# Optimization experiments

Hardware: AMD Instinct MI355X
Metric: run time of the kernel (lower is better)

Reference implementation:

```python
import jax, jax.numpy as jnp
import numpy as np

IN_CH, HID_CH = 32, 64
DILS = (1, 2, 4)


def _conv(x, w, b, dil, pad):
    # x: [B,C,H,W], w: [O,I,kh,kw]
    y = jax.lax.conv_general_dilated(
        x, w, window_strides=(1, 1), padding=[(pad, pad), (pad, pad)],
        rhs_dilation=(dil, dil), dimension_numbers=("NCHW", "OIHW", "NCHW"))
    return y + b[None, :, None, None]


def setup_inputs() -> dict:
    key = jax.random.key(0)
    ks = jax.random.split(key, 9)
    x_seq = jax.random.normal(ks[0], (4, 16, IN_CH, 64, 64), dtype=jnp.float32)
    params = {}
    ch = IN_CH
    for li, _ in enumerate(DILS):
        fan_in = (ch + HID_CH) * 9
        scale = 1.0 / np.sqrt(fan_in)
        params[f"gw{li}"] = jax.random.normal(ks[1 + 2 * li], (4 * HID_CH, ch + HID_CH, 3, 3), jnp.float32) * scale
        params[f"gb{li}"] = jnp.zeros((4 * HID_CH,), jnp.float32)
        ch = HID_CH
    # layer 0 residual 1x1 projection (in_ch != hid_ch)
    params["rw0"] = jax.random.normal(ks[7], (HID_CH, IN_CH, 1, 1), jnp.float32) * (1.0 / np.sqrt(IN_CH))
    params["rb0"] = jnp.zeros((HID_CH,), jnp.float32)
    return {"x_seq": x_seq, **params}


def _run_layer(seq, gw, gb, dil, res_fn):
    # seq: [B,T,C,H,W]
    B, T, C, H, W = seq.shape
    h0 = jnp.zeros((B, HID_CH, H, W), seq.dtype)
    c0 = jnp.zeros_like(h0)

    def step(carry, xt):
        h, c = carry
        g = _conv(jnp.concatenate([xt, h], axis=1), gw, gb, dil, dil)
        i, f, gg, o = jnp.split(g, 4, axis=1)
        c_new = jax.nn.sigmoid(f) * c + jax.nn.sigmoid(i) * jnp.tanh(gg)
        h_new = jax.nn.sigmoid(o) * jnp.tanh(c_new)
        h_out = h_new + res_fn(xt)  # residual added BEFORE next-step carry (matches torch)
        return (h_out, c_new), h_out

    xs = jnp.moveaxis(seq, 1, 0)  # [T,B,C,H,W]
    _, ys = jax.lax.scan(step, (h0, c0), xs)
    return jnp.moveaxis(ys, 0, 1)  # [B,T,hid,H,W]


def reference(x_seq, gw0, gb0, gw1, gb1, gw2, gb2, rw0, rb0):
    res0 = lambda xt: _conv(xt, rw0, rb0, 1, 0)
    ident = lambda xt: xt
    out = _run_layer(x_seq, gw0, gb0, DILS[0], res0)
    out = _run_layer(out, gw1, gb1, DILS[1], ident)
    out = _run_layer(out, gw2, gb2, DILS[2], ident)
    return out
```

## Files before the change

kernel.cpp:

```cpp
#include <hip/hip_runtime.h>
#include <hip/hip_bf16.h>

typedef __bf16 bf16;
typedef __bf16 bf16x8 __attribute__((ext_vector_type(8)));
typedef float f32x4 __attribute__((ext_vector_type(4)));
typedef unsigned short u16;
typedef unsigned short u16x8 __attribute__((ext_vector_type(8)));

#define TT 16
#define BB 4
#define HH 64
#define WW 64
#define HID 64

__device__ __forceinline__ float sigm_f(float x) { return 1.f / (1.f + __expf(-x)); }
__device__ __forceinline__ float tanh_f(float x) { return 1.f - 2.f / (__expf(2.f * x) + 1.f); }

__global__ void xpose_kernel(const float* __restrict__ x, bf16* __restrict__ xb) {
  int idx = blockIdx.x * blockDim.x + threadIdx.x;
  const int total = TT * BB * HH * WW * 32;
  if (idx >= total) return;
  int c = idx & 31;
  int xx = (idx >> 5) & 63;
  int y = (idx >> 11) & 63;
  int b = (idx >> 17) & 3;
  int t = idx >> 19;
  float v = x[((((b * TT + t) * 32 + c) * HH + y) * WW + xx)];
  xb[idx] = (bf16)v;
}

template <int CIN>
__global__ void wprep_kernel(const float* __restrict__ gw, bf16* __restrict__ bmat,
                             const float* __restrict__ rw, bf16* __restrict__ rwb) {
  const int K = CIN * 9;
  int idx = blockIdx.x * blockDim.x + threadIdx.x;
  int total = 256 * K;
  if (idx < total) {
    int n = idx / K;
    int kk = idx - n * K;
    int half = n >> 7, j = n & 127, gate = j >> 5, hcl = j & 31;
    int o = gate * 64 + half * 32 + hcl;
    int tap = kk / CIN, c = kk - tap * CIN;
    int ky = tap / 3, kx = tap - ky * 3;
    float v = gw[((o * CIN + c) * 3 + ky) * 3 + kx];
    int kt = kk >> 5, kin = kk & 31;
    bmat[(kt * 256 + n) * 32 + kin] = (bf16)v;
  } else if (rw != nullptr) {
    int r = idx - total;
    if (r < 64 * 32) rwb[r] = (bf16)rw[r];
  }
}

template <int L>
__global__ __launch_bounds__(512) void step_kernel(
    const bf16* __restrict__ xsrc, bf16* __restrict__ hbuf,
    const bf16* __restrict__ bmat, const float* __restrict__ gb,
    float* __restrict__ cbuf, const bf16* __restrict__ rwb,
    const float* __restrict__ rb, float* __restrict__ dout, int t) {
  constexpr int Cx = (L == 0) ? 32 : 64;
  constexpr int C = Cx + 64;
  constexpr int DIL = (L == 0) ? 1 : (L == 1 ? 2 : 4);
  constexpr int Wp = WW + 2 * DIL;
  constexpr int KT = (9 * C) / 32;
  constexpr int CT = C / 32;
  constexpr int HS = (L == 2) ? 2 : 16;

  __shared__ __align__(16) char smem[3 * Wp * C * 2 + 2 * 16384];
  char* alds = smem;
  char* blds = smem + 3 * Wp * C * 2;

  int bid = blockIdx.x;
  int b = bid >> 6, y = bid & 63;
  int tid = threadIdx.x;

  struct Bregs { u16x8 lo, hi; };
  auto loadB = [&](int kt) {
    Bregs r;
    const bf16* src = bmat + (size_t)kt * 256 * 32;
    r.lo = *(const u16x8*)(src + (size_t)tid * 8);
    r.hi = *(const u16x8*)(src + (size_t)(tid + 512) * 8);
    return r;
  };
  auto writeB = [&](const Bregs& r, int kt) {
    char* dst = blds + (kt & 1) * 16384;
    {
      int j = tid;
      int n = j >> 2, kin8 = (j & 3) * 8;
      int off = (n * 32 + kin8) * 2;
      off ^= (n & 7) << 4;
      *(u16x8*)(dst + off) = r.lo;
    }
    {
      int j = tid + 512;
      int n = j >> 2, kin8 = (j & 3) * 8;
      int off = (n * 32 + kin8) * 2;
      off ^= (n & 7) << 4;
      *(u16x8*)(dst + off) = r.hi;
    }
  };

  Bregs breg = loadB(0);

  {
    const int chunks = 3 * Wp * (C / 8);
    for (int i = tid; i < chunks; i += 512) {
      int cg = i % (C / 8);
      int rem = i / (C / 8);
      int col = rem % Wp;
      int row3 = rem / Wp;
      int c = cg * 8;
      int xs = col - DIL;
      int ys = y + (row3 - 1) * DIL;
      u16x8 v = {0, 0, 0, 0, 0, 0, 0, 0};
      if ((unsigned)xs < 64u && (unsigned)ys < 64u) {
        if (c < Cx) {
          v = *(const u16x8*)(xsrc + (size_t)(((t * BB + b) * HH + ys) * WW + xs) * Cx + c);
        } else if (t > 0) {
          int slot = (t - 1) & (HS - 1);
          v = *(const u16x8*)(hbuf + (size_t)(((slot * BB + b) * HH + ys) * WW + xs) * 64 + (c - Cx));
        }
      }
      int off = ((row3 * Wp + col) * C + c) * 2;
      off ^= (col & 7) << 4;
      *(u16x8*)(alds + off) = v;
    }
  }

  writeB(breg, 0);
  if (KT > 1) breg = loadB(1);

  int lane = tid & 63;
  int wave = tid >> 6;
  int pxg = wave & 3, half = wave >> 2;
  int pxbase = pxg * 16;
  int l15 = lane & 15, kgrp = lane >> 4;

  f32x4 acc[8];
  #pragma unroll
  for (int i = 0; i < 8; ++i) acc[i] = f32x4{0.f, 0.f, 0.f, 0.f};

  for (int kt = 0; kt < KT; ++kt) {
    __syncthreads();
    if (kt + 1 < KT) {
      writeB(breg, kt + 1);
      if (kt + 2 < KT) breg = loadB(kt + 2);
    }
    int tap = kt / CT;
    int cb = (kt % CT) * 32;
    int ky = tap / 3, kx = tap - ky * 3;
    int col = pxbase + l15 + kx * DIL;
    int aoff = ((ky * Wp + col) * C + cb + kgrp * 8) * 2;
    aoff ^= (col & 7) << 4;
    bf16x8 af = *(const bf16x8*)(alds + aoff);
    const char* bbase = blds + (kt & 1) * 16384;
    #pragma unroll
    for (int nt = 0; nt < 8; ++nt) {
      int n = half * 128 + nt * 16 + l15;
      int boff = (n * 32 + kgrp * 8) * 2;
      boff ^= (n & 7) << 4;
      bf16x8 bfr = *(const bf16x8*)(bbase + boff);
      acc[nt] = __builtin_amdgcn_mfma_f32_16x16x32_bf16(af, bfr, acc[nt], 0, 0, 0);
    }
  }

  #pragma unroll
  for (int hcu = 0; hcu < 2; ++hcu) {
    int hc = half * 32 + hcu * 16 + l15;
    float bi = gb[hc], bfg = gb[64 + hc], bgg = gb[128 + hc], bog = gb[192 + hc];
    f32x4 vi = acc[0 + hcu], vf = acc[2 + hcu], vg = acc[4 + hcu], vo = acc[6 + hcu];

    float rwv[32];
    float rbv = 0.f;
    if constexpr (L == 0) {
      rbv = rb[hc];
      const u16x8* rp = (const u16x8*)(rwb + hc * 32);
      #pragma unroll
      for (int q = 0; q < 4; ++q) {
        bf16x8 wb = *(const bf16x8*)(rp + q);
        #pragma unroll
        for (int e = 0; e < 8; ++e) rwv[q * 8 + e] = (float)wb[e];
      }
    }

    #pragma unroll
    for (int r = 0; r < 4; ++r) {
      int px = pxbase + kgrp * 4 + r;
      float giv = sigm_f(vi[r] + bi);
      float gfv = sigm_f(vf[r] + bfg);
      float ggv = tanh_f(vg[r] + bgg);
      float gov = sigm_f(vo[r] + bog);
      int cidx = ((b * HH + y) * WW + px) * 64 + hc;
      float cold = (t > 0) ? cbuf[cidx] : 0.f;
      float cn = gfv * cold + giv * ggv;
      cbuf[cidx] = cn;
      float hn = gov * tanh_f(cn);

      float res;
      int colc = px + DIL;
      if constexpr (L == 0) {
        float s = rbv;
        #pragma unroll
        for (int q = 0; q < 4; ++q) {
          int off = (((1 * Wp + colc) * C + q * 8) * 2) ^ ((colc & 7) << 4);
          bf16x8 xv = *(const bf16x8*)(alds + off);
          #pragma unroll
          for (int e = 0; e < 8; ++e) s += rwv[q * 8 + e] * (float)xv[e];
        }
        res = s;
      } else {
        int off = (((1 * Wp + colc) * C + hc) * 2) ^ ((colc & 7) << 4);
        res = (float)*(const bf16*)(alds + off);
      }
      float ho = hn + res;
      int hslot = t & (HS - 1);
      hbuf[(size_t)(((hslot * BB + b) * HH + y) * WW + px) * 64 + hc] = (bf16)ho;
      if constexpr (L == 2) {
        dout[(size_t)(((b * TT + t) * HID + hc) * HH + y) * WW + px] = ho;
      }
    }
  }
}

extern "C" void kernel_launch(void* const* d_in, const int* in_sizes, int n_in,
                              void* d_out, int out_size, void* d_ws, size_t ws_size,
                              hipStream_t stream) {
  const float* x_seq = (const float*)d_in[0];
  const float* gw0 = (const float*)d_in[1];
  const float* gb0 = (const float*)d_in[2];
  const float* gw1 = (const float*)d_in[3];
  const float* gb1 = (const float*)d_in[4];
  const float* gw2 = (const float*)d_in[5];
  const float* gb2 = (const float*)d_in[6];
  const float* rw0 = (const float*)d_in[7];
  const float* rb0 = (const float*)d_in[8];
  float* dout = (float*)d_out;

  char* ws = (char*)d_ws;
  size_t off = 0;
  auto carve = [&](size_t bytes) {
    char* p = ws + off;
    off += (bytes + 255) & ~(size_t)255;
    return p;
  };
  bf16* xb0 = (bf16*)carve((size_t)TT * BB * HH * WW * 32 * 2);
  bf16* seqA = (bf16*)carve((size_t)TT * BB * HH * WW * 64 * 2);
  bf16* seqB = (bf16*)carve((size_t)TT * BB * HH * WW * 64 * 2);
  bf16* hC = (bf16*)carve((size_t)2 * BB * HH * WW * 64 * 2);
  float* cbuf = (float*)carve((size_t)BB * HH * WW * 64 * 4);
  bf16* bm0 = (bf16*)carve((size_t)27 * 256 * 32 * 2);
  bf16* bm1 = (bf16*)carve((size_t)36 * 256 * 32 * 2);
  bf16* bm2 = (bf16*)carve((size_t)36 * 256 * 32 * 2);
  bf16* rwb = (bf16*)carve((size_t)64 * 32 * 2);

  {
    int total = TT * BB * HH * WW * 32;
    xpose_kernel<<<(total + 255) / 256, 256, 0, stream>>>(x_seq, xb0);
  }
  {
    int total = 256 * 96 * 9 + 64 * 32;
    wprep_kernel<96><<<(total + 255) / 256, 256, 0, stream>>>(gw0, bm0, rw0, rwb);
  }
  {
    int total = 256 * 128 * 9;
    wprep_kernel<128><<<(total + 255) / 256, 256, 0, stream>>>(gw1, bm1, nullptr, nullptr);
    wprep_kernel<128><<<(total + 255) / 256, 256, 0, stream>>>(gw2, bm2, nullptr, nullptr);
  }

  for (int t = 0; t < TT; ++t)
    step_kernel<0><<<BB * HH, 512, 0, stream>>>(xb0, seqA, bm0, gb0, cbuf, rwb, rb0, nullptr, t);
  for (int t = 0; t < TT; ++t)
    step_kernel<1><<<BB * HH, 512, 0, stream>>>(seqA, seqB, bm1, gb1, cbuf, nullptr, nullptr, nullptr, t);
  for (int t = 0; t < TT; ++t)
    step_kernel<2><<<BB * HH, 512, 0, stream>>>(seqB, hC, bm2, gb2, cbuf, nullptr, nullptr, dout, t);
}
```

Before: 1.262 ms.

## Keep gate weights in registers and restructure MFMA tiling per wave

Weight tiles are no longer staged through LDS with a barrier per k-step. Each wave now streams its own slice of B directly from global memory into a four-deep register ring, which removes the per-iteration __syncthreads. The wave tiling changes to two pixel M-tiles by four gate N-tiles, so each B fragment is reused across two MFMAs. The activation LDS layout is reorganized into 32-channel slabs, launch bounds request two blocks per CU, and the layer-2 output store is vectorized. In exchange, B is reloaded from global/L2 by every wave and register pressure rises.

```diff
diff --git a/kernel.cpp b/kernel.cpp
--- a/kernel.cpp
+++ b/kernel.cpp
@@ -38,8 +38,8 @@
   if (idx < total) {
     int n = idx / K;
     int kk = idx - n * K;
-    int half = n >> 7, j = n & 127, gate = j >> 5, hcl = j & 31;
-    int o = gate * 64 + half * 32 + hcl;
+    int q = n >> 6, j = n & 63, g = j >> 4, hcl = j & 15;
+    int o = g * 64 + q * 16 + hcl;
     int tap = kk / CIN, c = kk - tap * CIN;
     int ky = tap / 3, kx = tap - ky * 3;
     float v = gw[((o * CIN + c) * 3 + ky) * 3 + kx];
@@ -52,7 +52,7 @@
 }
 
 template <int L>
-__global__ __launch_bounds__(512) void step_kernel(
+__global__ __launch_bounds__(512, 2) void step_kernel(
     const bf16* __restrict__ xsrc, bf16* __restrict__ hbuf,
     const bf16* __restrict__ bmat, const float* __restrict__ gb,
     float* __restrict__ cbuf, const bf16* __restrict__ rwb,
@@ -65,50 +65,36 @@
   constexpr int CT = C / 32;
   constexpr int HS = (L == 2) ? 2 : 16;
 
-  __shared__ __align__(16) char smem[3 * Wp * C * 2 + 2 * 16384];
-  char* alds = smem;
-  char* blds = smem + 3 * Wp * C * 2;
+  __shared__ __align__(16) char alds[CT * 3 * Wp * 64];
 
   int bid = blockIdx.x;
   int b = bid >> 6, y = bid & 63;
   int tid = threadIdx.x;
-
-  struct Bregs { u16x8 lo, hi; };
-  auto loadB = [&](int kt) {
-    Bregs r;
-    const bf16* src = bmat + (size_t)kt * 256 * 32;
-    r.lo = *(const u16x8*)(src + (size_t)tid * 8);
-    r.hi = *(const u16x8*)(src + (size_t)(tid + 512) * 8);
-    return r;
+  int lane = tid & 63, wave = tid >> 6;
+  int l15 = lane & 15, kgrp = lane >> 4;
+  int pxg = wave >> 2, q = wave & 3;
+
+  const char* bmat_c = (const char*)bmat;
+  const int voffB = q * 4096 + l15 * 64 + kgrp * 16;
+
+  bf16x8 bfr[4][4];
+  auto loadB = [&](int slot, int kt) {
+    #pragma unroll
+    for (int g = 0; g < 4; ++g)
+      bfr[slot][g] = *(const bf16x8*)(bmat_c + (size_t)kt * 16384 + voffB + g * 1024);
   };
-  auto writeB = [&](const Bregs& r, int kt) {
-    char* dst = blds + (kt & 1) * 16384;
-    {
-      int j = tid;
-      int n = j >> 2, kin8 = (j & 3) * 8;
-      int off = (n * 32 + kin8) * 2;
-      off ^= (n & 7) << 4;
-      *(u16x8*)(dst + off) = r.lo;
-    }
-    {
-      int j = tid + 512;
-      int n = j >> 2, kin8 = (j & 3) * 8;
-      int off = (n * 32 + kin8) * 2;
-      off ^= (n & 7) << 4;
-      *(u16x8*)(dst + off) = r.hi;
-    }
-  };
-
-  Bregs breg = loadB(0);
+  loadB(0, 0);
+  loadB(1, 1);
 
   {
     const int chunks = 3 * Wp * (C / 8);
     for (int i = tid; i < chunks; i += 512) {
-      int cg = i % (C / 8);
-      int rem = i / (C / 8);
-      int col = rem % Wp;
-      int row3 = rem / Wp;
+      int col = i % Wp;
+      int rem = i / Wp;
+      int row3 = rem % 3;
+      int cg = rem / 3;
       int c = cg * 8;
+      int j = cg >> 2, sub = cg & 3;
       int xs = col - DIL;
       int ys = y + (row3 - 1) * DIL;
       u16x8 v = {0, 0, 0, 0, 0, 0, 0, 0};
@@ -120,71 +106,67 @@
           v = *(const u16x8*)(hbuf + (size_t)(((slot * BB + b) * HH + ys) * WW + xs) * 64 + (c - Cx));
         }
       }
-      int off = ((row3 * Wp + col) * C + c) * 2;
+      int off = ((j * 3 + row3) * Wp + col) * 64 + sub * 16;
       off ^= (col & 7) << 4;
       *(u16x8*)(alds + off) = v;
     }
   }
-
-  writeB(breg, 0);
-  if (KT > 1) breg = loadB(1);
-
-  int lane = tid & 63;
-  int wave = tid >> 6;
-  int pxg = wave & 3, half = wave >> 2;
-  int pxbase = pxg * 16;
-  int l15 = lane & 15, kgrp = lane >> 4;
-
-  f32x4 acc[8];
-  #pragma unroll
-  for (int i = 0; i < 8; ++i) acc[i] = f32x4{0.f, 0.f, 0.f, 0.f};
-
+  __syncthreads();
+
+  int abase[2][3];
+  #pragma unroll
+  for (int m = 0; m < 2; ++m)
+    #pragma unroll
+    for (int kx = 0; kx < 3; ++kx) {
+      int col = pxg * 32 + m * 16 + l15 + kx * DIL;
+      abase[m][kx] = (col * 64 + kgrp * 16) ^ ((col & 7) << 4);
+    }
+
+  f32x4 acc[2][4];
+  #pragma unroll
+  for (int m = 0; m < 2; ++m)
+    #pragma unroll
+    for (int g = 0; g < 4; ++g) acc[m][g] = f32x4{0.f, 0.f, 0.f, 0.f};
+
+  #pragma unroll
   for (int kt = 0; kt < KT; ++kt) {
-    __syncthreads();
-    if (kt + 1 < KT) {
-      writeB(breg, kt + 1);
-      if (kt + 2 < KT) breg = loadB(kt + 2);
-    }
+    if (kt + 2 < KT) loadB((kt + 2) & 3, kt + 2);
     int tap = kt / CT;
-    int cb = (kt % CT) * 32;
+    int j = kt - tap * CT;
     int ky = tap / 3, kx = tap - ky * 3;
-    int col = pxbase + l15 + kx * DIL;
-    int aoff = ((ky * Wp + col) * C + cb + kgrp * 8) * 2;
-    aoff ^= (col & 7) << 4;
-    bf16x8 af = *(const bf16x8*)(alds + aoff);
-    const char* bbase = blds + (kt & 1) * 16384;
-    #pragma unroll
-    for (int nt = 0; nt < 8; ++nt) {
-      int n = half * 128 + nt * 16 + l15;
-      int boff = (n * 32 + kgrp * 8) * 2;
-      boff ^= (n & 7) << 4;
-      bf16x8 bfr = *(const bf16x8*)(bbase + boff);
-      acc[nt] = __builtin_amdgcn_mfma_f32_16x16x32_bf16(af, bfr, acc[nt], 0, 0, 0);
-    }
-  }
-
-  #pragma unroll
-  for (int hcu = 0; hcu < 2; ++hcu) {
-    int hc = half * 32 + hcu * 16 + l15;
-    float bi = gb[hc], bfg = gb[64 + hc], bgg = gb[128 + hc], bog = gb[192 + hc];
-    f32x4 vi = acc[0 + hcu], vf = acc[2 + hcu], vg = acc[4 + hcu], vo = acc[6 + hcu];
-
-    float rwv[32];
-    float rbv = 0.f;
-    if constexpr (L == 0) {
-      rbv = rb[hc];
-      const u16x8* rp = (const u16x8*)(rwb + hc * 32);
+    int imm = ((j * 3 + ky) * Wp) * 64;
+    bf16x8 a0 = *(const bf16x8*)(alds + abase[0][kx] + imm);
+    bf16x8 a1 = *(const bf16x8*)(alds + abase[1][kx] + imm);
+    #pragma unroll
+    for (int g = 0; g < 4; ++g) {
+      acc[0][g] = __builtin_amdgcn_mfma_f32_16x16x32_bf16(a0, bfr[kt & 3][g], acc[0][g], 0, 0, 0);
+      acc[1][g] = __builtin_amdgcn_mfma_f32_16x16x32_bf16(a1, bfr[kt & 3][g], acc[1][g], 0, 0, 0);
+    }
+  }
+
+  int hc = q * 16 + l15;
+  float bi = gb[hc], bfg = gb[64 + hc], bgg = gb[128 + hc], bog = gb[192 + hc];
+
+  float rwv[32];
+  float rbv = 0.f;
+  if constexpr (L == 0) {
+    rbv = rb[hc];
+    const u16x8* rp = (const u16x8*)(rwb + hc * 32);
+    #pragma unroll
+    for (int p = 0; p < 4; ++p) {
+      bf16x8 wb = *(const bf16x8*)(rp + p);
       #pragma unroll
-      for (int q = 0; q < 4; ++q) {
-        bf16x8 wb = *(const bf16x8*)(rp + q);
-        #pragma unroll
-        for (int e = 0; e < 8; ++e) rwv[q * 8 + e] = (float)wb[e];
-      }
-    }
-
+      for (int e = 0; e < 8; ++e) rwv[p * 8 + e] = (float)wb[e];
+    }
+  }
+
+  #pragma unroll
+  for (int m = 0; m < 2; ++m) {
+    f32x4 vi = acc[m][0], vf = acc[m][1], vg = acc[m][2], vo = acc[m][3];
+    f32x4 hov;
     #pragma unroll
     for (int r = 0; r < 4; ++r) {
-      int px = pxbase + kgrp * 4 + r;
+      int px = pxg * 32 + m * 16 + kgrp * 4 + r;
       float giv = sigm_f(vi[r] + bi);
       float gfv = sigm_f(vf[r] + bfg);
       float ggv = tanh_f(vg[r] + bgg);
@@ -197,26 +179,30 @@
 
       float res;
       int colc = px + DIL;
+      int swz = (colc & 7) << 4;
       if constexpr (L == 0) {
         float s = rbv;
         #pragma unroll
-        for (int q = 0; q < 4; ++q) {
-          int off = (((1 * Wp + colc) * C + q * 8) * 2) ^ ((colc & 7) << 4);
+        for (int kc = 0; kc < 4; ++kc) {
+          int off = ((1 * Wp + colc) * 64 + kc * 16) ^ swz;
           bf16x8 xv = *(const bf16x8*)(alds + off);
           #pragma unroll
-          for (int e = 0; e < 8; ++e) s += rwv[q * 8 + e] * (float)xv[e];
+          for (int e = 0; e < 8; ++e) s += rwv[kc * 8 + e] * (float)xv[e];
         }
         res = s;
       } else {
-        int off = (((1 * Wp + colc) * C + hc) * 2) ^ ((colc & 7) << 4);
+        int jx = hc >> 5;
+        int off = (((jx * 3 + 1) * Wp + colc) * 64 + (hc & 31) * 2) ^ swz;
         res = (float)*(const bf16*)(alds + off);
       }
       float ho = hn + res;
+      hov[r] = ho;
       int hslot = t & (HS - 1);
       hbuf[(size_t)(((hslot * BB + b) * HH + y) * WW + px) * 64 + hc] = (bf16)ho;
-      if constexpr (L == 2) {
-        dout[(size_t)(((b * TT + t) * HID + hc) * HH + y) * WW + px] = ho;
-      }
+    }
+    if constexpr (L == 2) {
+      int px0 = pxg * 32 + m * 16 + kgrp * 4;
+      *(f32x4*)(dout + (size_t)(((b * TT + t) * HID + hc) * HH + y) * WW + px0) = hov;
     }
   }
 }
```

After: 1.246 ms. About the same (-1.3%).
